# Kernel optimization log

Measured on AMD Instinct MI355X. Metric: run time of the kernel, lower is better.

## Reference

```python
import jax, jax.numpy as jnp
import numpy as np
from jax import lax

TOP_K = 2

def setup_inputs() -> dict:
    key = jax.random.key(0)
    k1, k2, k3, k4 = jax.random.split(key, 4)
    T, H, I, E = 8192, 2048, 1408, 8
    x = jax.random.normal(k1, (T, H), dtype=jnp.float32)
    gate_w = jax.random.normal(k2, (E, H), dtype=jnp.float32) * 0.02
    gate_up_proj = jax.random.normal(k3, (E, 2 * I, H), dtype=jnp.float32) * 0.02
    down_proj = jax.random.normal(k4, (E, H, I), dtype=jnp.float32) * 0.02
    return {"x": x, "gate_w": gate_w, "gate_up_proj": gate_up_proj, "down_proj": down_proj}

def reference(x, gate_w, gate_up_proj, down_proj):
    E = gate_up_proj.shape[0]
    I = down_proj.shape[2]
    # router
    logits = x @ gate_w.T                                   # [T, E]
    probs = jax.nn.softmax(logits.astype(jnp.float32), axis=-1)
    topw, topi = lax.top_k(probs, TOP_K)                    # [T, K]
    topw = (topw / jnp.sum(topw, axis=-1, keepdims=True)).astype(x.dtype)
    # fused MoE: loop over small fixed expert count; dense GEMM per expert,
    # combine with per-token coefficient (0 if expert not selected).
    out = jnp.zeros_like(x)
    for e in range(E):
        coef = jnp.sum(jnp.where(topi == e, topw, 0.0), axis=-1)  # [T]
        gu = x @ gate_up_proj[e].T                                # [T, 2I]
        g, u = gu[:, :I], gu[:, I:]
        h = jax.nn.silu(g) * u                                    # [T, I]
        y = h @ down_proj[e].T                                    # [T, H]
        out = out + coef[:, None] * y
    return out
```

## Files before the change

kernel.cpp:

```cpp
#include <hip/hip_runtime.h>
#include <hip/hip_bf16.h>
#include <stdint.h>

#define T_TOK 8192
#define H_DIM 2048
#define I_DIM 1408
#define E_NUM 8
#define GU2   2816

typedef __attribute__((ext_vector_type(8))) short bf16x8;
typedef __attribute__((ext_vector_type(4))) float f32x4;

__device__ __forceinline__ void async_copy16(const void* g, void* lds) {
  __builtin_amdgcn_global_load_lds(
      (const __attribute__((address_space(1))) uint32_t*)g,
      (__attribute__((address_space(3))) uint32_t*)lds, 16, 0, 0);
}

__device__ __forceinline__ bf16x8 lds_read_swz(const short* tile, int row, int kcol) {
  int byte = (row << 7) + (kcol << 1);
  byte ^= (row & 7) << 4;
  return *(const bf16x8*)((const char*)tile + byte);
}

__device__ __forceinline__ float bfu2f(unsigned short u) {
  union { unsigned int i; float f; } v; v.i = ((unsigned int)u) << 16; return v.f;
}

__device__ __forceinline__ ushort4 cvt4(float4 v) {
  ushort4 o;
  __hip_bfloat16 b;
  b = __float2bfloat16(v.x); o.x = *reinterpret_cast<unsigned short*>(&b);
  b = __float2bfloat16(v.y); o.y = *reinterpret_cast<unsigned short*>(&b);
  b = __float2bfloat16(v.z); o.z = *reinterpret_cast<unsigned short*>(&b);
  b = __float2bfloat16(v.w); o.w = *reinterpret_cast<unsigned short*>(&b);
  return o;
}

__device__ __forceinline__ uint4 cvt8(float4 a, float4 b) {
  ushort4 x = cvt4(a), y = cvt4(b);
  uint4 r;
  r.x = (unsigned)x.x | ((unsigned)x.y << 16);
  r.y = (unsigned)x.z | ((unsigned)x.w << 16);
  r.z = (unsigned)y.x | ((unsigned)y.y << 16);
  r.w = (unsigned)y.z | ((unsigned)y.w << 16);
  return r;
}

__global__ __launch_bounds__(256) void cvtw_kernel(const float4* __restrict__ in,
                                                   uint4* __restrict__ out, int n8) {
  int j = blockIdx.x * blockDim.x + threadIdx.x;
  const int stride = gridDim.x * blockDim.x;
  for (; j + stride < n8; j += 2 * stride) {
    float4 a0 = in[2 * (size_t)j];
    float4 a1 = in[2 * (size_t)j + 1];
    float4 b0 = in[2 * (size_t)(j + stride)];
    float4 b1 = in[2 * (size_t)(j + stride) + 1];
    out[j] = cvt8(a0, a1);
    out[j + stride] = cvt8(b0, b1);
  }
  for (; j < n8; j += stride) {
    float4 a0 = in[2 * (size_t)j];
    float4 a1 = in[2 * (size_t)j + 1];
    out[j] = cvt8(a0, a1);
  }
}

__global__ __launch_bounds__(256) void gating_kernel(
    const float* __restrict__ x, const float* __restrict__ gw,
    int* __restrict__ invE, float* __restrict__ wslot,
    __hip_bfloat16* __restrict__ xb) {
  int wave = threadIdx.x >> 6, lane = threadIdx.x & 63;
  int t = blockIdx.x * 4 + wave;
  if (t >= T_TOK) return;
  const float4* xr = (const float4*)(x + (size_t)t * H_DIM);
  ushort4* xo = (ushort4*)((unsigned short*)xb + (size_t)t * H_DIM);
  float acc[E_NUM];
#pragma unroll
  for (int e = 0; e < E_NUM; ++e) acc[e] = 0.f;
#pragma unroll
  for (int i = 0; i < H_DIM / 256; ++i) {
    int c = i * 64 + lane;
    float4 xv = xr[c];
    xo[c] = cvt4(xv);
#pragma unroll
    for (int e = 0; e < E_NUM; ++e) {
      float4 g = ((const float4*)(gw + (size_t)e * H_DIM))[c];
      acc[e] += xv.x * g.x + xv.y * g.y + xv.z * g.z + xv.w * g.w;
    }
  }
#pragma unroll
  for (int e = 0; e < E_NUM; ++e) {
    float s = acc[e];
#pragma unroll
    for (int o = 32; o > 0; o >>= 1) s += __shfl_xor(s, o);
    acc[e] = s;
  }
  if (lane == 0) {
    int i1 = 0; float v1 = acc[0];
#pragma unroll
    for (int e = 1; e < E_NUM; ++e) if (acc[e] > v1) { v1 = acc[e]; i1 = e; }
    int i2 = -1; float v2 = -3.4e38f;
#pragma unroll
    for (int e = 0; e < E_NUM; ++e) if (e != i1 && acc[e] > v2) { v2 = acc[e]; i2 = e; }
    float p2 = expf(v2 - v1);
    float winv = 1.f / (1.f + p2);
    invE[2 * t] = i1;     wslot[2 * t] = winv;
    invE[2 * t + 1] = i2; wslot[2 * t + 1] = p2 * winv;
  }
}

__global__ __launch_bounds__(256) void buildlists_kernel(
    const int* __restrict__ invE, const float* __restrict__ wslot,
    int* __restrict__ cnt, int* __restrict__ basep,
    int* __restrict__ idx, float* __restrict__ wgt, int* __restrict__ invP)
{
  const int e = blockIdx.x;
  const int tid = threadIdx.x;
  const int wid = tid >> 6, lane = tid & 63;
  const int S = 2 * T_TOK;
  const int per = S / 256;
  const int c0 = tid * per;

  int cnt8[E_NUM];
#pragma unroll
  for (int i = 0; i < E_NUM; ++i) cnt8[i] = 0;
  for (int s = c0; s < c0 + per; ++s) cnt8[invE[s]]++;
  int mycnt = cnt8[e];

  __shared__ int sTot[E_NUM];
  __shared__ int sWave[4];
  if (tid < E_NUM) sTot[tid] = 0;
  __syncthreads();
#pragma unroll
  for (int i = 0; i < E_NUM; ++i)
    if (cnt8[i]) atomicAdd(&sTot[i], cnt8[i]);

  int v = mycnt;
#pragma unroll
  for (int o = 1; o < 64; o <<= 1) {
    int u = __shfl_up(v, o);
    if (lane >= o) v += u;
  }
  if (lane == 63) sWave[wid] = v;
  __syncthreads();
  int woff = 0;
#pragma unroll
  for (int w = 0; w < 4; ++w) if (w < wid) woff += sWave[w];
  int p = v - mycnt + woff;

  int base_e = 0;
#pragma unroll
  for (int i = 0; i < E_NUM; ++i) if (i < e) base_e += sTot[i];

  for (int s = c0; s < c0 + per; ++s) {
    if (invE[s] == e) {
      idx[e * T_TOK + p] = s >> 1;
      wgt[e * T_TOK + p] = wslot[s];
      invP[s] = p;
      ++p;
    }
  }
  if (tid == 0) { cnt[e] = sTot[e]; basep[e] = base_e; }
}

__global__ __launch_bounds__(256, 3) void gemm1_kernel(
    const __hip_bfloat16* __restrict__ xb, const __hip_bfloat16* __restrict__ wb1,
    const int* __restrict__ cnt, const int* __restrict__ base, const int* __restrict__ idx,
    __hip_bfloat16* __restrict__ hbuf)
{
  int lin = blockIdx.x;
  int swz = (lin & 7) * 440 + (lin >> 3);
  int e = swz / 440; int rem = swz - e * 440;
  int by = rem / 22; int bx = rem - by * 22;
  const int ne = cnt[e];
  const int rowbase = by * 128;
  if (rowbase >= ne) return;
  const int jbase = bx * 64;
  const int hb = base[e];

  __shared__ short sA[128 * 64];
  __shared__ short sB[128 * 64];

  const int tid = threadIdx.x, wid = tid >> 6, lane = tid & 63;
  const int wr = wid >> 1, wc = wid & 1;
  const int l15 = lane & 15, lhi = lane >> 4;
  const int* idx_e = idx + e * T_TOK;
  const char* xs = (const char*)xb;
  const char* w1s = (const char*)wb1 + (size_t)e * GU2 * H_DIM * 2;

  const int cb = (((tid & 7) ^ ((tid >> 3) & 7)) << 4);
  const char* aSrc[4]; const char* bSrc[4];
#pragma unroll
  for (int q = 0; q < 4; ++q) {
    int r = q * 32 + (tid >> 3);
    int i = rowbase + r; if (i > ne - 1) i = ne - 1;
    aSrc[q] = xs + (size_t)idx_e[i] * (H_DIM * 2) + cb;
    int wrow = (r < 64) ? (jbase + r) : (I_DIM + jbase + (r - 64));
    bSrc[q] = w1s + (size_t)wrow * (H_DIM * 2) + cb;
  }

  f32x4 accg[4][2], accu[4][2];
#pragma unroll
  for (int m = 0; m < 4; ++m)
#pragma unroll
    for (int n = 0; n < 2; ++n) { accg[m][n] = (f32x4){0,0,0,0}; accu[m][n] = (f32x4){0,0,0,0}; }

  const int NK = H_DIM / 64;

  for (int kt = 0; kt < NK; ++kt) {
    const size_t koff = (size_t)kt * 128;
#pragma unroll
    for (int q = 0; q < 4; ++q) {
      async_copy16(aSrc[q] + koff, (char*)sA + q * 4096 + wid * 1024);
      async_copy16(bSrc[q] + koff, (char*)sB + q * 4096 + wid * 1024);
    }
    __syncthreads();

    bf16x8 a[4][2], bg[2][2], bu[2][2];
#pragma unroll
    for (int m = 0; m < 4; ++m)
#pragma unroll
      for (int ks = 0; ks < 2; ++ks)
        a[m][ks] = lds_read_swz(sA, wr * 64 + m * 16 + l15, ks * 32 + (lhi << 3));
#pragma unroll
    for (int n = 0; n < 2; ++n)
#pragma unroll
      for (int ks = 0; ks < 2; ++ks) {
        bg[n][ks] = lds_read_swz(sB, wc * 32 + n * 16 + l15, ks * 32 + (lhi << 3));
        bu[n][ks] = lds_read_swz(sB, 64 + wc * 32 + n * 16 + l15, ks * 32 + (lhi << 3));
      }
    __builtin_amdgcn_s_setprio(1);
#pragma unroll
    for (int m = 0; m < 4; ++m)
#pragma unroll
      for (int n = 0; n < 2; ++n)
#pragma unroll
        for (int ks = 0; ks < 2; ++ks) {
          accg[m][n] = __builtin_amdgcn_mfma_f32_16x16x32_bf16(a[m][ks], bg[n][ks], accg[m][n], 0, 0, 0);
          accu[m][n] = __builtin_amdgcn_mfma_f32_16x16x32_bf16(a[m][ks], bu[n][ks], accu[m][n], 0, 0, 0);
        }
    __builtin_amdgcn_s_setprio(0);
    __syncthreads();
  }

#pragma unroll
  for (int m = 0; m < 4; ++m) {
#pragma unroll
    for (int n = 0; n < 2; ++n) {
      int col = jbase + wc * 32 + n * 16 + l15;
#pragma unroll
      for (int j = 0; j < 4; ++j) {
        int rl = wr * 64 + m * 16 + lhi * 4 + j;
        int i = rowbase + rl;
        if (i < ne) {
          float g = accg[m][n][j], u = accu[m][n][j];
          float hv = (g / (1.f + __expf(-g))) * u;
          hbuf[(size_t)(hb + i) * I_DIM + col] = __float2bfloat16(hv);
        }
      }
    }
  }
}

__global__ __launch_bounds__(256, 3) void gemm2_kernel(
    const __hip_bfloat16* __restrict__ hbuf, const __hip_bfloat16* __restrict__ wb2,
    const int* __restrict__ cnt, const int* __restrict__ base,
    const float* __restrict__ wgt, __hip_bfloat16* __restrict__ ybuf)
{
  int lin = blockIdx.x;
  int swz = (lin & 7) * 320 + (lin >> 3);
  int e = swz / 320; int rem = swz - e * 320;
  int by = rem >> 4; int bx = rem & 15;
  const int ne = cnt[e];
  const int rowbase = by * 128;
  if (rowbase >= ne) return;
  const int nbase = bx * 128;
  const int hb = base[e];

  __shared__ short sA[128 * 64];
  __shared__ short sB[128 * 64];
  __shared__ float sW[128];

  const int tid = threadIdx.x, wid = tid >> 6, lane = tid & 63;
  const int wr = wid >> 1, wc = wid & 1;
  const int l15 = lane & 15, lhi = lane >> 4;
  const float* wgt_e = wgt + e * T_TOK;
  const char* hs = (const char*)hbuf;
  const char* w2s = (const char*)wb2 + (size_t)e * H_DIM * I_DIM * 2;

  if (tid < 128) {
    int i = rowbase + tid;
    sW[tid] = (i < ne) ? wgt_e[i] : 0.f;
  }

  const int cb = (((tid & 7) ^ ((tid >> 3) & 7)) << 4);
  const char* aSrc[4]; const char* bSrc[4];
#pragma unroll
  for (int q = 0; q < 4; ++q) {
    int r = q * 32 + (tid >> 3);
    int i = rowbase + r; if (i > ne - 1) i = ne - 1;
    aSrc[q] = hs + (size_t)(hb + i) * (I_DIM * 2) + cb;
    bSrc[q] = w2s + (size_t)(nbase + r) * (I_DIM * 2) + cb;
  }

  f32x4 acc[4][4];
#pragma unroll
  for (int m = 0; m < 4; ++m)
#pragma unroll
    for (int n = 0; n < 4; ++n) acc[m][n] = (f32x4){0, 0, 0, 0};

  const int NK = I_DIM / 64;

  for (int kt = 0; kt < NK; ++kt) {
    const size_t koff = (size_t)kt * 128;
#pragma unroll
    for (int q = 0; q < 4; ++q) {
      async_copy16(aSrc[q] + koff, (char*)sA + q * 4096 + wid * 1024);
      async_copy16(bSrc[q] + koff, (char*)sB + q * 4096 + wid * 1024);
    }
    __syncthreads();

    bf16x8 a[4][2], b[4][2];
#pragma unroll
    for (int m = 0; m < 4; ++m)
#pragma unroll
      for (int ks = 0; ks < 2; ++ks)
        a[m][ks] = lds_read_swz(sA, wr * 64 + m * 16 + l15, ks * 32 + (lhi << 3));
#pragma unroll
    for (int n = 0; n < 4; ++n)
#pragma unroll
      for (int ks = 0; ks < 2; ++ks)
        b[n][ks] = lds_read_swz(sB, wc * 64 + n * 16 + l15, ks * 32 + (lhi << 3));
    __builtin_amdgcn_s_setprio(1);
#pragma unroll
    for (int m = 0; m < 4; ++m)
#pragma unroll
      for (int n = 0; n < 4; ++n)
#pragma unroll
        for (int ks = 0; ks < 2; ++ks)
          acc[m][n] = __builtin_amdgcn_mfma_f32_16x16x32_bf16(a[m][ks], b[n][ks], acc[m][n], 0, 0, 0);
    __builtin_amdgcn_s_setprio(0);
    __syncthreads();
  }

#pragma unroll
  for (int m = 0; m < 4; ++m)
#pragma unroll
    for (int n = 0; n < 4; ++n) {
      int col = nbase + wc * 64 + n * 16 + l15;
#pragma unroll
      for (int j = 0; j < 4; ++j) {
        int rl = wr * 64 + m * 16 + lhi * 4 + j;
        if (rowbase + rl < ne) {
          float y = acc[m][n][j] * sW[rl];
          ybuf[(size_t)(hb + rowbase + rl) * H_DIM + col] = __float2bfloat16(y);
        }
      }
    }
}

__global__ __launch_bounds__(256) void combine_kernel(
    const __hip_bfloat16* __restrict__ ybuf, const int* __restrict__ base,
    const int* __restrict__ invE, const int* __restrict__ invP,
    float* __restrict__ out)
{
  int t = blockIdx.x;
  int s1 = base[invE[2 * t]] + invP[2 * t];
  int s2 = base[invE[2 * t + 1]] + invP[2 * t + 1];
  const ushort* y1 = (const ushort*)ybuf + (size_t)s1 * H_DIM;
  const ushort* y2 = (const ushort*)ybuf + (size_t)s2 * H_DIM;
  float* o = out + (size_t)t * H_DIM;
#pragma unroll
  for (int c0 = 0; c0 < H_DIM; c0 += 256 * 4) {
    int c = c0 + threadIdx.x * 4;
    ushort4 a = *(const ushort4*)(y1 + c);
    ushort4 b = *(const ushort4*)(y2 + c);
    float4 r;
    r.x = bfu2f(a.x) + bfu2f(b.x);
    r.y = bfu2f(a.y) + bfu2f(b.y);
    r.z = bfu2f(a.z) + bfu2f(b.z);
    r.w = bfu2f(a.w) + bfu2f(b.w);
    *(float4*)(o + c) = r;
  }
}

extern "C" void kernel_launch(void* const* d_in, const int* in_sizes, int n_in,
                              void* d_out, int out_size, void* d_ws, size_t ws_size,
                              hipStream_t stream) {
  const float* x  = (const float*)d_in[0];
  const float* gw = (const float*)d_in[1];
  const float* w1 = (const float*)d_in[2];
  const float* w2 = (const float*)d_in[3];
  float* out = (float*)d_out;

  char* ws = (char*)d_ws;
  size_t o = 0;
  __hip_bfloat16* xb   = (__hip_bfloat16*)(ws + o); o += (size_t)T_TOK * H_DIM * 2;
  __hip_bfloat16* wb1  = (__hip_bfloat16*)(ws + o); o += (size_t)E_NUM * GU2 * H_DIM * 2;
  __hip_bfloat16* wb2  = (__hip_bfloat16*)(ws + o); o += (size_t)E_NUM * H_DIM * I_DIM * 2;
  __hip_bfloat16* hbuf = (__hip_bfloat16*)(ws + o); o += (size_t)2 * T_TOK * I_DIM * 2;
  int*   idx   = (int*)(ws + o);   o += (size_t)E_NUM * T_TOK * 4;
  float* wgt   = (float*)(ws + o); o += (size_t)E_NUM * T_TOK * 4;
  int*   invE  = (int*)(ws + o);   o += (size_t)2 * T_TOK * 4;
  int*   invP  = (int*)(ws + o);   o += (size_t)2 * T_TOK * 4;
  float* wslot = (float*)(ws + o); o += (size_t)2 * T_TOK * 4;
  int*   cnt   = (int*)(ws + o);   o += 64;
  int*   base  = (int*)(ws + o);   o += 64;
  __hip_bfloat16* ybuf = (__hip_bfloat16*)ws;

  cvtw_kernel<<<2048, 256, 0, stream>>>((const float4*)w1, (uint4*)wb1, (E_NUM * GU2 * H_DIM) / 8);
  cvtw_kernel<<<2048, 256, 0, stream>>>((const float4*)w2, (uint4*)wb2, (E_NUM * H_DIM * I_DIM) / 8);
  gating_kernel<<<T_TOK / 4, 256, 0, stream>>>(x, gw, invE, wslot, xb);
  buildlists_kernel<<<E_NUM, 256, 0, stream>>>(invE, wslot, cnt, base, idx, wgt, invP);

  gemm1_kernel<<<dim3(3520), 256, 0, stream>>>(xb, wb1, cnt, base, idx, hbuf);
  gemm2_kernel<<<dim3(2560), 256, 0, stream>>>(hbuf, wb2, cnt, base, wgt, ybuf);

  combine_kernel<<<T_TOK, 256, 0, stream>>>(ybuf, base, invE, invP, out);
}
```

Baseline: 478.5 us.

## Fuse weight conversions into gating and gemm1 launches for overlap

The w1 fp32-to-bf16 conversion now runs as extra blocks of a combined prep kernel alongside gating, and the w2 conversion runs as extra blocks appended to the gemm1 grid. This removes two separate launches and lets memory-bound conversion overlap with gating and with the compute-bound GEMM1. The risk is that gemm1 blocks now share the GPU with bandwidth-heavy conversion blocks, and block scheduling order determines how much overlap actually happens.

```diff
diff --git a/kernel.cpp b/kernel.cpp
--- a/kernel.cpp
+++ b/kernel.cpp
@@ -47,10 +47,11 @@
   return r;
 }
 
-__global__ __launch_bounds__(256) void cvtw_kernel(const float4* __restrict__ in,
-                                                   uint4* __restrict__ out, int n8) {
-  int j = blockIdx.x * blockDim.x + threadIdx.x;
-  const int stride = gridDim.x * blockDim.x;
+__device__ __forceinline__ void cvt_body(const float4* __restrict__ in,
+                                         uint4* __restrict__ out, int n8,
+                                         int b, int nblocks) {
+  int j = b * 256 + threadIdx.x;
+  const int stride = nblocks * 256;
   for (; j + stride < n8; j += 2 * stride) {
     float4 a0 = in[2 * (size_t)j];
     float4 a1 = in[2 * (size_t)j + 1];
@@ -66,12 +67,19 @@
   }
 }
 
-__global__ __launch_bounds__(256) void gating_kernel(
+__global__ __launch_bounds__(256) void prep_kernel(
     const float* __restrict__ x, const float* __restrict__ gw,
+    const float4* __restrict__ w1, uint4* __restrict__ wb1,
     int* __restrict__ invE, float* __restrict__ wslot,
-    __hip_bfloat16* __restrict__ xb) {
+    __hip_bfloat16* __restrict__ xb)
+{
+  int b = blockIdx.x;
+  if (b >= 2048) {
+    cvt_body(w1, wb1, (E_NUM * GU2 * H_DIM) / 8, b - 2048, 2048);
+    return;
+  }
   int wave = threadIdx.x >> 6, lane = threadIdx.x & 63;
-  int t = blockIdx.x * 4 + wave;
+  int t = b * 4 + wave;
   if (t >= T_TOK) return;
   const float4* xr = (const float4*)(x + (size_t)t * H_DIM);
   ushort4* xo = (ushort4*)((unsigned short*)xb + (size_t)t * H_DIM);
@@ -166,10 +174,18 @@
 
 __global__ __launch_bounds__(256, 3) void gemm1_kernel(
     const __hip_bfloat16* __restrict__ xb, const __hip_bfloat16* __restrict__ wb1,
+    const float4* __restrict__ w2, uint4* __restrict__ wb2,
     const int* __restrict__ cnt, const int* __restrict__ base, const int* __restrict__ idx,
     __hip_bfloat16* __restrict__ hbuf)
 {
+  __shared__ short sA[128 * 64];
+  __shared__ short sB[128 * 64];
+
   int lin = blockIdx.x;
+  if (lin >= 3520) {
+    cvt_body(w2, wb2, (E_NUM * H_DIM * I_DIM) / 8, lin - 3520, 2048);
+    return;
+  }
   int swz = (lin & 7) * 440 + (lin >> 3);
   int e = swz / 440; int rem = swz - e * 440;
   int by = rem / 22; int bx = rem - by * 22;
@@ -178,9 +194,6 @@
   if (rowbase >= ne) return;
   const int jbase = bx * 64;
   const int hb = base[e];
-
-  __shared__ short sA[128 * 64];
-  __shared__ short sB[128 * 64];
 
   const int tid = threadIdx.x, wid = tid >> 6, lane = tid & 63;
   const int wr = wid >> 1, wc = wid & 1;
@@ -409,12 +422,12 @@
   int*   base  = (int*)(ws + o);   o += 64;
   __hip_bfloat16* ybuf = (__hip_bfloat16*)ws;
 
-  cvtw_kernel<<<2048, 256, 0, stream>>>((const float4*)w1, (uint4*)wb1, (E_NUM * GU2 * H_DIM) / 8);
-  cvtw_kernel<<<2048, 256, 0, stream>>>((const float4*)w2, (uint4*)wb2, (E_NUM * H_DIM * I_DIM) / 8);
-  gating_kernel<<<T_TOK / 4, 256, 0, stream>>>(x, gw, invE, wslot, xb);
+  prep_kernel<<<4096, 256, 0, stream>>>(x, gw, (const float4*)w1, (uint4*)wb1,
+                                        invE, wslot, xb);
   buildlists_kernel<<<E_NUM, 256, 0, stream>>>(invE, wslot, cnt, base, idx, wgt, invP);
 
-  gemm1_kernel<<<dim3(3520), 256, 0, stream>>>(xb, wb1, cnt, base, idx, hbuf);
+  gemm1_kernel<<<dim3(5568), 256, 0, stream>>>(xb, wb1, (const float4*)w2, (uint4*)wb2,
+                                               cnt, base, idx, hbuf);
   gemm2_kernel<<<dim3(2560), 256, 0, stream>>>(hbuf, wb2, cnt, base, wgt, ybuf);
 
   combine_kernel<<<T_TOK, 256, 0, stream>>>(ybuf, base, invE, invP, out);
```

New measurement: 472.2 us. About the same (-1.3%).
